# Kernel tuning notes

Hardware: AMD Instinct MI355X
Metric: run time of the kernel (lower is better)

The kernel has to match this reference:

```python
import jax, jax.numpy as jnp
import numpy as np

B, S, E, H = 2, 2048, 2048, 16
D = E // H  # head_dim = 128


def rotate_half(x):
    x1, x2 = jnp.split(x, 2, axis=-1)
    return jnp.concatenate([-x2, x1], axis=-1)


def rope_sincos(seq_len, dim):
    inv_freq = 1.0 / (10000.0 ** (jnp.arange(0, dim, 2, dtype=jnp.float32) / dim))
    t = jnp.arange(seq_len, dtype=jnp.float32)
    freqs = jnp.outer(t, inv_freq)            # [S, D/2]
    emb = jnp.concatenate([freqs, freqs], -1)  # [S, D]
    return jnp.sin(emb), jnp.cos(emb)


def apply_rope(x, sin, cos):
    # x: [B, S, H, D]; sin/cos: [S, D] -> [1, S, 1, D]
    sin = sin[None, :, None, :]
    cos = cos[None, :, None, :]
    return x * cos + rotate_half(x) * sin


def setup_inputs() -> dict:
    key = jax.random.key(0)
    k1, k2 = jax.random.split(key)
    x = jax.random.normal(k1, (B, S, E), dtype=jnp.float32)
    # causal boolean mask [B, 1, S, S]
    mask = jnp.broadcast_to(jnp.tril(jnp.ones((S, S), dtype=bool))[None, None], (B, 1, S, S))
    # fused QKV projection weight (hk.Linear, no bias): [E, 3E]
    W_qkv = jax.random.normal(k2, (E, 3 * E), dtype=jnp.float32) / np.sqrt(E)
    return {"x": x, "mask": mask, "W_qkv": W_qkv}


def reference(x, mask, W_qkv):
    seq_len = x.shape[1]
    qkv = x @ W_qkv                               # [B, S, 3E]
    q, k, v = jnp.split(qkv, 3, axis=-1)
    q = q.reshape(-1, seq_len, H, D)
    k = k.reshape(-1, seq_len, H, D)
    v = v.reshape(-1, seq_len, H, D)
    sin, cos = rope_sincos(seq_len, D)
    q = apply_rope(q, sin, cos)
    k = apply_rope(k, sin, cos)
    attn = jnp.einsum('bqhd,bkhd->bhqk', q, k) / jnp.sqrt(jnp.float32(D))
    m = jnp.broadcast_to(mask, (mask.shape[0], H, seq_len, k.shape[1]))
    attn = jnp.where(m, attn, -jnp.inf)
    attn = jax.nn.softmax(attn, axis=-1)
    out = jnp.einsum('bhqk,bkhd->bqhd', attn, v)
    return out.reshape(-1, seq_len, H * D)
```

## Files before the change

kernel.cpp:

```cpp
#include <hip/hip_runtime.h>

typedef __bf16 bf16;
typedef __bf16 bf16x8 __attribute__((ext_vector_type(8)));
typedef __bf16 bf16x4 __attribute__((ext_vector_type(4)));
typedef float f32x4 __attribute__((ext_vector_type(4)));

#define MFMA16(a, b, c) __builtin_amdgcn_mfma_f32_16x16x32_bf16(a, b, c, 0, 0, 0)

#define Bq 2
#define Sq 2048
#define Eq 2048
#define Hq 16
#define Dq 128
#define N3E 6144

#define GLOAD_LDS16(gp, lp) \
  __builtin_amdgcn_global_load_lds( \
      (const __attribute__((address_space(1))) void*)(gp), \
      (__attribute__((address_space(3))) void*)(lp), 16, 0, 0)

__device__ __forceinline__ bf16 f2bf(float f) {
  unsigned u = __builtin_bit_cast(unsigned, f);
  u += 0x7FFFu + ((u >> 16) & 1u);
  unsigned short h = (unsigned short)(u >> 16);
  return __builtin_bit_cast(bf16, h);
}
__device__ __forceinline__ float bf2f(bf16 b) {
  unsigned short h = __builtin_bit_cast(unsigned short, b);
  return __builtin_bit_cast(float, (unsigned)h << 16);
}

__global__ __launch_bounds__(256) void convert_x(const float* __restrict__ x,
                                                 bf16* __restrict__ xb) {
  const size_t i = ((size_t)blockIdx.x * 256 + threadIdx.x) * 8;
  float4 a = *(const float4*)(x + i);
  float4 b = *(const float4*)(x + i + 4);
  bf16x8 o;
  o[0] = f2bf(a.x); o[1] = f2bf(a.y); o[2] = f2bf(a.z); o[3] = f2bf(a.w);
  o[4] = f2bf(b.x); o[5] = f2bf(b.y); o[6] = f2bf(b.z); o[7] = f2bf(b.w);
  *(bf16x8*)(xb + i) = o;
}

__global__ __launch_bounds__(256) void convert_wt(const float* __restrict__ w,
                                                  bf16* __restrict__ wt) {
  __shared__ __align__(16) bf16 T[64][72];
  const int tid = threadIdx.x;
  const int kb = blockIdx.x & 31;
  const int nb = blockIdx.x >> 5;
  const int k0 = kb * 64, n0 = nb * 64;
  {
    const int kr = tid >> 4, nc = (tid & 15) * 4;
#pragma unroll
    for (int p = 0; p < 4; ++p) {
      const int k = kr + p * 16;
      float4 v = *(const float4*)(w + (size_t)(k0 + k) * N3E + n0 + nc);
      T[nc + 0][k] = f2bf(v.x);
      T[nc + 1][k] = f2bf(v.y);
      T[nc + 2][k] = f2bf(v.z);
      T[nc + 3][k] = f2bf(v.w);
    }
  }
  __syncthreads();
#pragma unroll
  for (int q = 0; q < 2; ++q) {
    const int id = q * 256 + tid;
    const int n = id >> 3, ch = id & 7;
    bf16x8 v = *(const bf16x8*)&T[n][ch * 8];
    *(bf16x8*)(wt + (size_t)(n0 + n) * Eq + k0 + ch * 8) = v;
  }
}

__global__ __launch_bounds__(256) void rope_table(float2* __restrict__ tbl) {
  const int i = blockIdx.x * 256 + threadIdx.x;
  const int s = i >> 6, d = i & 63;
  const float freq = __expf(-(float)d * 0.14391157f);
  const float ang = (float)s * freq;
  float sv, cv;
  __sincosf(ang, &sv, &cv);
  tbl[i] = make_float2(cv, sv);
}

__global__ __launch_bounds__(512, 2) void gemm_qkv(
    const bf16* __restrict__ xb, const bf16* __restrict__ wt,
    const float2* __restrict__ tbl, bf16* __restrict__ qws,
    bf16* __restrict__ kws, bf16* __restrict__ vtws) {
  __shared__ __align__(16) bf16 LDS[3 * 24576];

  const int tid = threadIdx.x;
  const int lane = tid & 63, wv = tid >> 6;
  const int q4 = lane >> 4, c = lane & 15;
  const int wm = (wv >> 2) * 64;
  const int wn = (wv & 3) * 64;

  const int bid = blockIdx.x;
  const int wg = (bid & 7) * 96 + (bid >> 3);
  const int m0 = (wg / 24) * 128;
  const int n0 = (wg % 24) * 256;

  f32x4 acc[4][4];
#pragma unroll
  for (int i = 0; i < 4; ++i)
#pragma unroll
    for (int j = 0; j < 4; ++j) acc[i][j] = {0.f, 0.f, 0.f, 0.f};

  const int NT = Eq / 64;

  auto stage = [&](int t, int st) {
    bf16* ab = LDS + st * 24576;
    bf16* bb = ab + 8192;
    const int k0 = t * 64;
#pragma unroll
    for (int it = 0; it < 2; ++it) {
      const int slot = it * 512 + tid;
      const int row = slot >> 3, kch = slot & 7;
      const int kcs = kch ^ (row & 7);
      GLOAD_LDS16(xb + (size_t)(m0 + row) * Eq + k0 + kcs * 8, ab + slot * 8);
    }
#pragma unroll
    for (int it = 0; it < 4; ++it) {
      const int slot = it * 512 + tid;
      const int row = slot >> 3, kch = slot & 7;
      const int kcs = kch ^ (row & 7);
      GLOAD_LDS16(wt + (size_t)(n0 + row) * Eq + k0 + kcs * 8, bb + slot * 8);
    }
  };

  stage(0, 0);
  stage(1, 1);
  asm volatile("s_waitcnt vmcnt(6)" ::: "memory");
  __builtin_amdgcn_s_barrier();

  int stC = 0;
#pragma unroll 1
  for (int t = 0; t < NT; ++t) {
    if (t + 2 < NT) {
      int ss = stC + 2;
      if (ss >= 3) ss -= 3;
      stage(t + 2, ss);
    }
    const bf16* A = LDS + stC * 24576;
    const bf16* Bb = A + 8192;
#pragma unroll
    for (int kk = 0; kk < 64; kk += 32) {
      const int bch = kk >> 3;
      bf16x8 af[4], bfr[4];
#pragma unroll
      for (int i = 0; i < 4; ++i)
        af[i] = *(const bf16x8*)
            &A[(wm + i * 16 + c) * 64 + ((bch + q4) ^ (c & 7)) * 8];
#pragma unroll
      for (int j = 0; j < 4; ++j)
        bfr[j] = *(const bf16x8*)
            &Bb[(wn + j * 16 + c) * 64 + ((bch + q4) ^ (c & 7)) * 8];
      __builtin_amdgcn_s_setprio(1);
#pragma unroll
      for (int i = 0; i < 4; ++i)
#pragma unroll
        for (int j = 0; j < 4; ++j)
          acc[i][j] = MFMA16(af[i], bfr[j], acc[i][j]);
      __builtin_amdgcn_s_setprio(0);
    }
    if (t + 1 < NT) {
      if (t + 2 < NT) asm volatile("s_waitcnt vmcnt(6)" ::: "memory");
      else            asm volatile("s_waitcnt vmcnt(0)" ::: "memory");
      __builtin_amdgcn_s_barrier();
    }
    stC = stC == 2 ? 0 : stC + 1;
  }
  __syncthreads();

  const int t3 = n0 >> 11;
  const int b = m0 >> 11;
  const int s0 = m0 & 2047;
  const int h0 = (n0 & 2047) >> 7;

  bf16* E = LDS;

  if (t3 == 2) {
#pragma unroll 1
    for (int hh = 0; hh < 2; ++hh) {
      if (((wv & 3) >> 1) == hh) {
#pragma unroll
        for (int i = 0; i < 4; ++i)
#pragma unroll
          for (int j = 0; j < 4; ++j) {
            bf16x4 pv;
            pv[0] = f2bf(acc[i][j][0]); pv[1] = f2bf(acc[i][j][1]);
            pv[2] = f2bf(acc[i][j][2]); pv[3] = f2bf(acc[i][j][3]);
            *(bf16x4*)&E[((wn & 127) + j * 16 + c) * 136 + wm + i * 16 +
                         q4 * 4] = pv;
          }
      }
      __syncthreads();
      bf16* vbase = vtws + ((size_t)(b * Hq + h0 + hh) * Dq) * Sq + s0;
#pragma unroll
      for (int p = 0; p < 4; ++p) {
        const int id = p * 512 + tid;
        const int d = id >> 4, ch = id & 15;
        bf16x8 v = *(const bf16x8*)&E[d * 136 + ch * 8];
        *(bf16x8*)&vbase[(size_t)d * Sq + ch * 8] = v;
      }
      __syncthreads();
    }
  } else {
#pragma unroll 1
    for (int hh = 0; hh < 2; ++hh) {
      if (((wv & 3) >> 1) == hh) {
#pragma unroll
        for (int i = 0; i < 4; ++i)
#pragma unroll
          for (int j = 0; j < 4; ++j)
#pragma unroll
            for (int rr = 0; rr < 4; ++rr)
              E[(wm + i * 16 + q4 * 4 + rr) * 136 + (wn & 127) + j * 16 + c] =
                  f2bf(acc[i][j][rr]);
      }
      __syncthreads();
      bf16* hd = ((t3 == 0) ? qws : kws) +
                 ((size_t)(b * Hq + h0 + hh) * Sq + s0) * Dq;
#pragma unroll
      for (int p = 0; p < 2; ++p) {
        const int row = p * 64 + (tid >> 3);
        const int dlow = (tid & 7) * 8;
        const int s = s0 + row;
        bf16x8 lo = *(const bf16x8*)&E[row * 136 + dlow];
        bf16x8 hi = *(const bf16x8*)&E[row * 136 + 64 + dlow];
        const float2* tb = tbl + (size_t)s * 64 + dlow;
        bf16x8 olo, ohi;
#pragma unroll
        for (int e = 0; e < 8; ++e) {
          const float cv = tb[e].x, sv = tb[e].y;
          const float x1 = bf2f(lo[e]), x2 = bf2f(hi[e]);
          olo[e] = f2bf(x1 * cv - x2 * sv);
          ohi[e] = f2bf(x2 * cv + x1 * sv);
        }
        *(bf16x8*)&hd[(size_t)row * Dq + dlow] = olo;
        *(bf16x8*)&hd[(size_t)row * Dq + 64 + dlow] = ohi;
      }
      __syncthreads();
    }
  }
}

__global__ __launch_bounds__(256, 2) void attn_kernel(
    const bf16* __restrict__ qws, const bf16* __restrict__ kws,
    const bf16* __restrict__ vtws, float* __restrict__ out) {
  __shared__ __align__(16) bf16 Kld[2][8192];
  __shared__ __align__(16) bf16 Vld[2][8192];
  __shared__ __align__(16) bf16 Plds[4][16][72];

  const int tid = threadIdx.x, lane = tid & 63, wave = tid >> 6;
  const int q4 = lane >> 4, c = lane & 15;
  const int h = blockIdx.y, b = blockIdx.z;
  const int qt = b ? blockIdx.x : (15 - blockIdx.x);
  const size_t bh = (size_t)(b * Hq + h);
  const bf16* qbase = qws + bh * Sq * Dq;
  const bf16* kbase = kws + bh * Sq * Dq;
  const bf16* vbase = vtws + bh * Dq * Sq;
  const int q0 = qt * 128 + wave * 32;
  const float kSc = 0.08838834764831845f * 1.4426950408889634f;

  bf16x8 qf[2][4];
#pragma unroll
  for (int g = 0; g < 2; ++g)
#pragma unroll
    for (int ks = 0; ks < 4; ++ks)
      qf[g][ks] = *(const bf16x8*)
          &qbase[(size_t)(q0 + g * 16 + c) * Dq + ks * 32 + q4 * 8];

  f32x4 Ot[2][8];
  float m_i[2], l_i[2];
#pragma unroll
  for (int g = 0; g < 2; ++g) {
#pragma unroll
    for (int dj = 0; dj < 8; ++dj) Ot[g][dj] = {0.f, 0.f, 0.f, 0.f};
    m_i[g] = -1e30f; l_i[g] = 0.f;
  }

  const int nchunks = 2 * qt + 2;

#pragma unroll
  for (int it = 0; it < 4; ++it) {
    const int slot = it * 256 + tid;
    GLOAD_LDS16(kbase + (size_t)(slot & 63) * Dq + (slot >> 6) * 8,
                &Kld[0][slot * 8]);
    GLOAD_LDS16(vbase + (size_t)(slot & 127) * Sq + (slot >> 7) * 8,
                &Vld[0][slot * 8]);
  }
  __syncthreads();

  for (int kb = 0; kb < nchunks; ++kb) {
    const int buf = kb & 1;
    if (kb + 1 < nchunks) {
      const int nb = buf ^ 1;
      const int koff = (kb + 1) * 64;
#pragma unroll
      for (int it = 0; it < 4; ++it) {
        const int slot = it * 256 + tid;
        GLOAD_LDS16(kbase + (size_t)(koff + (slot & 63)) * Dq + (slot >> 6) * 8,
                    &Kld[nb][slot * 8]);
        GLOAD_LDS16(vbase + (size_t)(slot & 127) * Sq + koff + (slot >> 7) * 8,
                    &Vld[nb][slot * 8]);
      }
    }
    const bool masked = (kb >= 2 * qt);
#pragma unroll
    for (int g = 0; g < 2; ++g) {
      const int qg = q0 + g * 16 + c;
      f32x4 st[4];
#pragma unroll
      for (int j8 = 0; j8 < 4; ++j8) st[j8] = {0.f, 0.f, 0.f, 0.f};
#pragma unroll
      for (int ks = 0; ks < 4; ++ks) {
        const bf16x8 qv = qf[g][ks];
#pragma unroll
        for (int j8 = 0; j8 < 4; ++j8) {
          const bf16x8 kv = *(const bf16x8*)
              &Kld[buf][((ks * 4 + q4) * 64 + j8 * 16 + c) * 8];
          st[j8] = MFMA16(kv, qv, st[j8]);
        }
      }
      if (masked) {
        const int kb64 = kb * 64 + q4 * 4;
#pragma unroll
        for (int j8 = 0; j8 < 4; ++j8)
#pragma unroll
          for (int rr = 0; rr < 4; ++rr)
            if (kb64 + j8 * 16 + rr > qg) st[j8][rr] = -1e30f;
      }
      float mloc = -1e30f;
#pragma unroll
      for (int j8 = 0; j8 < 4; ++j8)
#pragma unroll
        for (int rr = 0; rr < 4; ++rr) mloc = fmaxf(mloc, st[j8][rr]);
      mloc = fmaxf(mloc, __shfl_xor(mloc, 16, 64));
      mloc = fmaxf(mloc, __shfl_xor(mloc, 32, 64));
      const float mn = fmaxf(m_i[g], mloc);
      const float alpha = exp2f((m_i[g] - mn) * kSc);
      m_i[g] = mn;
      float ssum = 0.f;
#pragma unroll
      for (int j8 = 0; j8 < 4; ++j8)
#pragma unroll
        for (int rr = 0; rr < 4; ++rr) {
          const float p = exp2f((st[j8][rr] - mn) * kSc);
          st[j8][rr] = p;
          ssum += p;
        }
      ssum += __shfl_xor(ssum, 16, 64);
      ssum += __shfl_xor(ssum, 32, 64);
      l_i[g] = l_i[g] * alpha + ssum;
#pragma unroll
      for (int dj = 0; dj < 8; ++dj) Ot[g][dj] *= alpha;
#pragma unroll
      for (int j8 = 0; j8 < 4; ++j8) {
        bf16x4 pk;
        pk[0] = f2bf(st[j8][0]); pk[1] = f2bf(st[j8][1]);
        pk[2] = f2bf(st[j8][2]); pk[3] = f2bf(st[j8][3]);
        *(bf16x4*)&Plds[wave][c][j8 * 16 + q4 * 4] = pk;
      }
#pragma unroll
      for (int ks = 0; ks < 2; ++ks) {
        const bf16x8 pv = *(const bf16x8*)&Plds[wave][c][ks * 32 + q4 * 8];
#pragma unroll
        for (int dj = 0; dj < 8; ++dj) {
          const bf16x8 vv = *(const bf16x8*)
              &Vld[buf][((ks * 4 + q4) * 128 + dj * 16 + c) * 8];
          Ot[g][dj] = MFMA16(vv, pv, Ot[g][dj]);
        }
      }
    }
    __syncthreads();
  }

#pragma unroll
  for (int g = 0; g < 2; ++g) {
    const float inv = 1.0f / l_i[g];
    float* orow = out + ((size_t)b * Sq + q0 + g * 16 + c) * Eq + h * Dq;
#pragma unroll
    for (int dj = 0; dj < 8; ++dj) {
      float4 o;
      o.x = Ot[g][dj][0] * inv; o.y = Ot[g][dj][1] * inv;
      o.z = Ot[g][dj][2] * inv; o.w = Ot[g][dj][3] * inv;
      *(float4*)&orow[dj * 16 + q4 * 4] = o;
    }
  }
}

extern "C" void kernel_launch(void* const* d_in, const int* in_sizes, int n_in,
                              void* d_out, int out_size, void* d_ws,
                              size_t ws_size, hipStream_t stream) {
  const float* x = (const float*)d_in[0];
  const float* w = (const float*)d_in[2];
  float* out = (float*)d_out;

  const size_t nX = (size_t)Bq * Sq * Eq;
  const size_t nW = (size_t)Eq * N3E;
  const size_t perT = (size_t)Bq * Hq * Sq * Dq;

  bf16* xb = (bf16*)d_ws;
  bf16* wt = xb + nX;
  bf16* qws = wt + nW;
  bf16* kws = qws + perT;
  bf16* vtws = kws + perT;
  float2* tbl = (float2*)(vtws + perT);

  convert_x<<<nX / (256 * 8), 256, 0, stream>>>(x, xb);
  convert_wt<<<(Eq / 64) * (N3E / 64), 256, 0, stream>>>(w, wt);
  rope_table<<<(Sq * 64) / 256, 256, 0, stream>>>(tbl);

  gemm_qkv<<<768, 512, 0, stream>>>(xb, wt, tbl, qws, kws, vtws);

  dim3 g3(Sq / 128, Hq, Bq);
  attn_kernel<<<g3, 256, 0, stream>>>(qws, kws, vtws, out);
}
```

Before: 374.1 us.

## Merge prep kernels, skip unchanged-max rescale, raise MFMA priority in attention

Folds the x conversion, weight transpose-conversion and RoPE table kernels into one launch that picks its role by block index, removing two kernel launches and their gaps. In the attention kernel, the online-softmax rescale of the output accumulator and running sum now runs only when some lane's row maximum grows. MFMA sections are wrapped in s_setprio to favour matrix issue. A small hoist of c&7 is also made in the GEMM. The conditional rescale adds a wave-wide vote and a branch, and the fused prep kernel reserves LDS even for blocks that do not use it.

```diff
diff --git a/kernel.cpp b/kernel.cpp
--- a/kernel.cpp
+++ b/kernel.cpp
@@ -30,54 +30,57 @@
   return __builtin_bit_cast(float, (unsigned)h << 16);
 }
 
-__global__ __launch_bounds__(256) void convert_x(const float* __restrict__ x,
-                                                 bf16* __restrict__ xb) {
-  const size_t i = ((size_t)blockIdx.x * 256 + threadIdx.x) * 8;
-  float4 a = *(const float4*)(x + i);
-  float4 b = *(const float4*)(x + i + 4);
-  bf16x8 o;
-  o[0] = f2bf(a.x); o[1] = f2bf(a.y); o[2] = f2bf(a.z); o[3] = f2bf(a.w);
-  o[4] = f2bf(b.x); o[5] = f2bf(b.y); o[6] = f2bf(b.z); o[7] = f2bf(b.w);
-  *(bf16x8*)(xb + i) = o;
-}
-
-__global__ __launch_bounds__(256) void convert_wt(const float* __restrict__ w,
-                                                  bf16* __restrict__ wt) {
+__global__ __launch_bounds__(256) void prep(const float* __restrict__ x,
+                                            bf16* __restrict__ xb,
+                                            const float* __restrict__ w,
+                                            bf16* __restrict__ wt,
+                                            float2* __restrict__ tbl) {
   __shared__ __align__(16) bf16 T[64][72];
   const int tid = threadIdx.x;
-  const int kb = blockIdx.x & 31;
-  const int nb = blockIdx.x >> 5;
-  const int k0 = kb * 64, n0 = nb * 64;
-  {
-    const int kr = tid >> 4, nc = (tid & 15) * 4;
-#pragma unroll
-    for (int p = 0; p < 4; ++p) {
-      const int k = kr + p * 16;
-      float4 v = *(const float4*)(w + (size_t)(k0 + k) * N3E + n0 + nc);
-      T[nc + 0][k] = f2bf(v.x);
-      T[nc + 1][k] = f2bf(v.y);
-      T[nc + 2][k] = f2bf(v.z);
-      T[nc + 3][k] = f2bf(v.w);
-    }
-  }
-  __syncthreads();
-#pragma unroll
-  for (int q = 0; q < 2; ++q) {
-    const int id = q * 256 + tid;
-    const int n = id >> 3, ch = id & 7;
-    bf16x8 v = *(const bf16x8*)&T[n][ch * 8];
-    *(bf16x8*)(wt + (size_t)(n0 + n) * Eq + k0 + ch * 8) = v;
-  }
-}
-
-__global__ __launch_bounds__(256) void rope_table(float2* __restrict__ tbl) {
-  const int i = blockIdx.x * 256 + threadIdx.x;
-  const int s = i >> 6, d = i & 63;
-  const float freq = __expf(-(float)d * 0.14391157f);
-  const float ang = (float)s * freq;
-  float sv, cv;
-  __sincosf(ang, &sv, &cv);
-  tbl[i] = make_float2(cv, sv);
+  const int bidx = blockIdx.x;
+
+  if (bidx < 4096) {
+    const size_t i = ((size_t)bidx * 256 + tid) * 8;
+    float4 a = *(const float4*)(x + i);
+    float4 b = *(const float4*)(x + i + 4);
+    bf16x8 o;
+    o[0] = f2bf(a.x); o[1] = f2bf(a.y); o[2] = f2bf(a.z); o[3] = f2bf(a.w);
+    o[4] = f2bf(b.x); o[5] = f2bf(b.y); o[6] = f2bf(b.z); o[7] = f2bf(b.w);
+    *(bf16x8*)(xb + i) = o;
+  } else if (bidx < 4096 + 3072) {
+    const int b2 = bidx - 4096;
+    const int kb = b2 & 31;
+    const int nb = b2 >> 5;
+    const int k0 = kb * 64, n0 = nb * 64;
+    {
+      const int kr = tid >> 4, nc = (tid & 15) * 4;
+#pragma unroll
+      for (int p = 0; p < 4; ++p) {
+        const int k = kr + p * 16;
+        float4 v = *(const float4*)(w + (size_t)(k0 + k) * N3E + n0 + nc);
+        T[nc + 0][k] = f2bf(v.x);
+        T[nc + 1][k] = f2bf(v.y);
+        T[nc + 2][k] = f2bf(v.z);
+        T[nc + 3][k] = f2bf(v.w);
+      }
+    }
+    __syncthreads();
+#pragma unroll
+    for (int q = 0; q < 2; ++q) {
+      const int id = q * 256 + tid;
+      const int n = id >> 3, ch = id & 7;
+      bf16x8 v = *(const bf16x8*)&T[n][ch * 8];
+      *(bf16x8*)(wt + (size_t)(n0 + n) * Eq + k0 + ch * 8) = v;
+    }
+  } else {
+    const int i = (bidx - 7168) * 256 + tid;
+    const int s = i >> 6, d = i & 63;
+    const float freq = __expf(-(float)d * 0.14391157f);
+    const float ang = (float)s * freq;
+    float sv, cv;
+    __sincosf(ang, &sv, &cv);
+    tbl[i] = make_float2(cv, sv);
+  }
 }
 
 __global__ __launch_bounds__(512, 2) void gemm_qkv(
@@ -91,6 +94,7 @@
   const int q4 = lane >> 4, c = lane & 15;
   const int wm = (wv >> 2) * 64;
   const int wn = (wv & 3) * 64;
+  const int cx = c & 7;
 
   const int bid = blockIdx.x;
   const int wg = (bid & 7) * 96 + (bid >> 3);
@@ -147,11 +151,11 @@
 #pragma unroll
       for (int i = 0; i < 4; ++i)
         af[i] = *(const bf16x8*)
-            &A[(wm + i * 16 + c) * 64 + ((bch + q4) ^ (c & 7)) * 8];
+            &A[(wm + i * 16 + c) * 64 + ((bch + q4) ^ cx) * 8];
 #pragma unroll
       for (int j = 0; j < 4; ++j)
         bfr[j] = *(const bf16x8*)
-            &Bb[(wn + j * 16 + c) * 64 + ((bch + q4) ^ (c & 7)) * 8];
+            &Bb[(wn + j * 16 + c) * 64 + ((bch + q4) ^ cx) * 8];
       __builtin_amdgcn_s_setprio(1);
 #pragma unroll
       for (int i = 0; i < 4; ++i)
@@ -310,6 +314,7 @@
       f32x4 st[4];
 #pragma unroll
       for (int j8 = 0; j8 < 4; ++j8) st[j8] = {0.f, 0.f, 0.f, 0.f};
+      __builtin_amdgcn_s_setprio(1);
 #pragma unroll
       for (int ks = 0; ks < 4; ++ks) {
         const bf16x8 qv = qf[g][ks];
@@ -320,6 +325,7 @@
           st[j8] = MFMA16(kv, qv, st[j8]);
         }
       }
+      __builtin_amdgcn_s_setprio(0);
       if (masked) {
         const int kb64 = kb * 64 + q4 * 4;
 #pragma unroll
@@ -335,9 +341,15 @@
         for (int rr = 0; rr < 4; ++rr) mloc = fmaxf(mloc, st[j8][rr]);
       mloc = fmaxf(mloc, __shfl_xor(mloc, 16, 64));
       mloc = fmaxf(mloc, __shfl_xor(mloc, 32, 64));
-      const float mn = fmaxf(m_i[g], mloc);
-      const float alpha = exp2f((m_i[g] - mn) * kSc);
-      m_i[g] = mn;
+      float mn = m_i[g];
+      if (__any(mloc > mn)) {
+        mn = fmaxf(mn, mloc);
+        const float alpha = exp2f((m_i[g] - mn) * kSc);
+        m_i[g] = mn;
+        l_i[g] *= alpha;
+#pragma unroll
+        for (int dj = 0; dj < 8; ++dj) Ot[g][dj] *= alpha;
+      }
       float ssum = 0.f;
 #pragma unroll
       for (int j8 = 0; j8 < 4; ++j8)
@@ -349,9 +361,7 @@
         }
       ssum += __shfl_xor(ssum, 16, 64);
       ssum += __shfl_xor(ssum, 32, 64);
-      l_i[g] = l_i[g] * alpha + ssum;
-#pragma unroll
-      for (int dj = 0; dj < 8; ++dj) Ot[g][dj] *= alpha;
+      l_i[g] += ssum;
 #pragma unroll
       for (int j8 = 0; j8 < 4; ++j8) {
         bf16x4 pk;
@@ -359,6 +369,7 @@
         pk[2] = f2bf(st[j8][2]); pk[3] = f2bf(st[j8][3]);
         *(bf16x4*)&Plds[wave][c][j8 * 16 + q4 * 4] = pk;
       }
+      __builtin_amdgcn_s_setprio(1);
 #pragma unroll
       for (int ks = 0; ks < 2; ++ks) {
         const bf16x8 pv = *(const bf16x8*)&Plds[wave][c][ks * 32 + q4 * 8];
@@ -369,6 +380,7 @@
           Ot[g][dj] = MFMA16(vv, pv, Ot[g][dj]);
         }
       }
+      __builtin_amdgcn_s_setprio(0);
     }
     __syncthreads();
   }
@@ -405,9 +417,7 @@
   bf16* vtws = kws + perT;
   float2* tbl = (float2*)(vtws + perT);
 
-  convert_x<<<nX / (256 * 8), 256, 0, stream>>>(x, xb);
-  convert_wt<<<(Eq / 64) * (N3E / 64), 256, 0, stream>>>(w, wt);
-  rope_table<<<(Sq * 64) / 256, 256, 0, stream>>>(tbl);
+  prep<<<7680, 256, 0, stream>>>(x, xb, w, wt, tbl);
 
   gemm_qkv<<<768, 512, 0, stream>>>(xb, wt, tbl, qws, kws, vtws);
 
```

Measured after the change: 374.8 us. No clear change (+0.2%).
